# Optimization experiments

Measured on AMD Instinct MI355X. Metric: run time of the kernel, lower is better.

## Reference

```python
import jax, jax.numpy as jnp
import numpy as np

ALPHA = 0.7
NUM_HEADS = 12
NUM_KV_HEADS = 6
HEAD_DIM = 64
ROPE_BASE = 10000.0


def ternary_quantize(w):
    thr = ALPHA * jnp.mean(jnp.abs(w))
    return jnp.sign(w) * (jnp.abs(w) >= thr).astype(w.dtype)


def bitlinear(x, w):
    # forward: F.linear(x, ternary(w)) * mean(|w|)
    scale = jnp.mean(jnp.abs(w))
    qw = ternary_quantize(w)
    return (x @ qw.T) * scale


def rope_tables(seq_len, dim, dtype):
    inv_freq = 1.0 / (ROPE_BASE ** (jnp.arange(0, dim, 2, dtype=jnp.float32) / dim))
    t = jnp.arange(seq_len, dtype=jnp.float32)
    freqs = jnp.outer(t, inv_freq)            # [S, dim/2]
    emb = jnp.concatenate([freqs, freqs], -1)  # [S, dim]
    return jnp.cos(emb).astype(dtype), jnp.sin(emb).astype(dtype)


def rotate_half(x):
    x1, x2 = jnp.split(x, 2, axis=-1)
    return jnp.concatenate([-x2, x1], axis=-1)


def setup_inputs() -> dict:
    key = jax.random.key(0)
    ks = jax.random.split(key, 5)
    B, S, H = 2, 2048, 768
    return {
        "hidden_states": jax.random.normal(ks[0], (B, S, H), jnp.float32),
        "Wq": jax.random.normal(ks[1], (768, 768), jnp.float32) * 0.02,
        "Wk": jax.random.normal(ks[2], (384, 768), jnp.float32) * 0.02,
        "Wv": jax.random.normal(ks[3], (384, 768), jnp.float32) * 0.02,
        "Wo": jax.random.normal(ks[4], (768, 768), jnp.float32) * 0.02,
    }


def reference(hidden_states, Wq, Wk, Wv, Wo):
    B, S, H = hidden_states.shape
    nh, nkv, hd = NUM_HEADS, NUM_KV_HEADS, HEAD_DIM
    groups = nh // nkv

    q = bitlinear(hidden_states, Wq).reshape(B, S, nh, hd).transpose(0, 2, 1, 3)
    k = bitlinear(hidden_states, Wk).reshape(B, S, nkv, hd).transpose(0, 2, 1, 3)
    v = bitlinear(hidden_states, Wv).reshape(B, S, nkv, hd).transpose(0, 2, 1, 3)

    cos, sin = rope_tables(S, hd, hidden_states.dtype)  # [S, hd]
    cos = cos[None, None]  # [1,1,S,hd]
    sin = sin[None, None]
    q = q * cos + rotate_half(q) * sin
    k = k * cos + rotate_half(k) * sin

    # GQA: expand kv heads to full head count
    k = jnp.repeat(k, groups, axis=1)  # [B, nh, S, hd]
    v = jnp.repeat(v, groups, axis=1)

    scale = 1.0 / jnp.sqrt(jnp.asarray(hd, hidden_states.dtype))
    scores = jnp.einsum("bhsd,bhtd->bhst", q, k) * scale
    attn = jax.nn.softmax(scores, axis=-1)
    out = jnp.einsum("bhst,bhtd->bhsd", attn, v)
    out = out.transpose(0, 2, 1, 3).reshape(B, S, H)
    return bitlinear(out, Wo)
```

## Files before the change

kernel.cpp:

```cpp
#include <hip/hip_runtime.h>
#include <cmath>

typedef unsigned short u16;
typedef unsigned int u32;
typedef __bf16 bf16x2 __attribute__((ext_vector_type(2)));
typedef __bf16 bf16x8 __attribute__((ext_vector_type(8)));
typedef float f32x16 __attribute__((ext_vector_type(16)));

#define NQ (768*768)
#define NK (384*768)

__device__ __forceinline__ u16 f2bf(float f) {
  u32 u = __float_as_uint(f);
  u32 r = (u + 0x7FFFu + ((u >> 16) & 1u)) >> 16;
  return (u16)r;
}
__device__ __forceinline__ u32 packbf(float a, float b) {
#if __has_builtin(__builtin_amdgcn_cvt_pk_bf16_f32)
  bf16x2 v = __builtin_amdgcn_cvt_pk_bf16_f32(a, b);
  u32 r; __builtin_memcpy(&r, &v, 4); return r;
#else
  return (u32)f2bf(a) | ((u32)f2bf(b) << 16);
#endif
}
__device__ __forceinline__ float fexp2(float x) {
#if __has_builtin(__builtin_amdgcn_exp2f)
  return __builtin_amdgcn_exp2f(x);
#else
  return exp2f(x);
#endif
}
__device__ __forceinline__ bf16x8 ldfrag(const u16* p) { bf16x8 v; __builtin_memcpy(&v, p, 16); return v; }
__device__ __forceinline__ f32x16 mfma32_(bf16x8 a, bf16x8 b, f32x16 c) {
  return __builtin_amdgcn_mfma_f32_32x32x16_bf16(a, b, c, 0, 0, 0);
}

__device__ __forceinline__ int fidx(int r, int k) {
  return (r >> 5) * 24576 + (k >> 4) * 512 + ((r & 31) + 32 * ((k >> 3) & 1)) * 8 + (k & 7);
}
__device__ __forceinline__ int kidx(int b6kvh, int s, int d) {
  return b6kvh * 131072 + (s >> 5) * 2048 + (d >> 4) * 512 +
         ((s & 31) + 32 * ((d >> 3) & 1)) * 8 + (d & 7);
}
__device__ __forceinline__ int qidx(int b, int s, int h, int d) {
  return ((b * 64 + (s >> 5)) * 12 + h) * 2048 + (d >> 4) * 512 +
         ((s & 31) + 32 * ((d >> 3) & 1)) * 8 + (d & 7);
}
__device__ __forceinline__ int vidx(int b6kvh, int d, int p) {
  return b6kvh * 131072 + (p >> 6) * 4096 + (d >> 5) * 2048 + ((p >> 4) & 3) * 512 +
         ((d & 31) + 32 * ((p >> 3) & 1)) * 8 + (p & 7);
}

__global__ __launch_bounds__(256) void abssum_kernel(const float* __restrict__ wq, const float* __restrict__ wk,
                                                     const float* __restrict__ wv, const float* __restrict__ wo,
                                                     float* __restrict__ sums) {
  int which = blockIdx.y;
  const float* w = (which == 0) ? wq : (which == 1) ? wk : (which == 2) ? wv : wo;
  int n4 = ((which == 0 || which == 3) ? NQ : NK) >> 2;
  const float4* w4 = (const float4*)w;
  float s = 0.f;
  for (int i = blockIdx.x * blockDim.x + threadIdx.x; i < n4; i += gridDim.x * blockDim.x) {
    float4 v = w4[i];
    s += fabsf(v.x) + fabsf(v.y) + fabsf(v.z) + fabsf(v.w);
  }
  for (int off = 32; off; off >>= 1) s += __shfl_down(s, off);
  __shared__ float ls[4];
  if ((threadIdx.x & 63) == 0) ls[threadIdx.x >> 6] = s;
  __syncthreads();
  if (threadIdx.x == 0) atomicAdd(&sums[which], ls[0] + ls[1] + ls[2] + ls[3]);
}

__global__ __launch_bounds__(256) void prep_kernel(const float* __restrict__ wq, const float* __restrict__ wk,
                                                   const float* __restrict__ wv, const float* __restrict__ wo,
                                                   const float* __restrict__ sums, const float* __restrict__ x,
                                                   u16* __restrict__ qw, u16* __restrict__ woq,
                                                   u16* __restrict__ xb) {
  int i = blockIdx.x * blockDim.x + threadIdx.x;
  if (i < 221184) {
    int n = i / 96, k8 = i - n * 96;
    const float* src; float th; u16* dst; int nd;
    if (n < 768)       { src = wq + n * 768;          th = 0.7f * sums[0] * (1.f / NQ); dst = qw;  nd = n; }
    else if (n < 1152) { src = wk + (n - 768) * 768;  th = 0.7f * sums[1] * (1.f / NK); dst = qw;  nd = n; }
    else if (n < 1536) { src = wv + (n - 1152) * 768; th = 0.7f * sums[2] * (1.f / NK); dst = qw;  nd = n; }
    else               { src = wo + (n - 1536) * 768; th = 0.7f * sums[3] * (1.f / NQ); dst = woq; nd = n - 1536; }
    const float4* sp = (const float4*)(src + k8 * 8);
    float4 v0 = sp[0], v1 = sp[1];
    float e[8] = {v0.x, v0.y, v0.z, v0.w, v1.x, v1.y, v1.z, v1.w};
    u16 o[8];
#pragma unroll
    for (int j = 0; j < 8; j++)
      o[j] = f2bf((fabsf(e[j]) >= th) ? ((e[j] > 0.f) ? 1.f : -1.f) : 0.f);
    __builtin_memcpy(dst + fidx(nd, k8 * 8), o, 16);
  } else {
    int j = i - 221184;
    int m = j / 96, k8 = j - m * 96;
    const float4* xp = (const float4*)(x + m * 768 + k8 * 8);
    float4 v0 = xp[0], v1 = xp[1];
    u16 o[8] = { f2bf(v0.x), f2bf(v0.y), f2bf(v0.z), f2bf(v0.w),
                 f2bf(v1.x), f2bf(v1.y), f2bf(v1.z), f2bf(v1.w) };
    __builtin_memcpy(xb + fidx(m, k8 * 8), o, 16);
  }
}

__global__ __launch_bounds__(256, 3) void gemm_qkv_kernel(const u16* __restrict__ xb, const u16* __restrict__ qw,
                                                          const float* __restrict__ sums,
                                                          u16* __restrict__ qb, u16* __restrict__ kb,
                                                          u16* __restrict__ vT) {
  int tn = blockIdx.x, tm = blockIdx.y;
  int t = threadIdx.x, lane = t & 63, w = t >> 6, c = lane & 31, g2 = lane >> 5;
  int wm = w & 1, wn = w >> 1;
  const u16* abase = xb + (tm * 2 + wm) * 24576 + lane * 8;
  const u16* bbase0 = qw + (tn * 4 + wn * 2) * 24576 + lane * 8;
  const u16* bbase1 = bbase0 + 24576;
  f32x16 acc[2]; acc[0] = (f32x16)0.f; acc[1] = (f32x16)0.f;
  for (int kk = 0; kk < 48; kk += 4) {
#pragma unroll
    for (int ks = 0; ks < 4; ks++) {
      bf16x8 af = ldfrag(abase + (kk + ks) * 512);
      bf16x8 b0 = ldfrag(bbase0 + (kk + ks) * 512);
      bf16x8 b1 = ldfrag(bbase1 + (kk + ks) * 512);
      acc[0] = mfma32_(af, b0, acc[0]);
      acc[1] = mfma32_(af, b1, acc[1]);
    }
  }
  float sq = sums[0] * (1.f / NQ) * 0.180336880111120f;
  float sk = sums[1] * (1.f / NK);
  float sv = sums[2] * (1.f / NK);
  int mb = tm * 64 + wm * 32 + 4 * g2;
  if (tn < 9) {
    float sc = (tn < 6) ? sq : sk;
    int head = (tn < 6) ? (tn * 2 + wn) : ((tn - 6) * 2 + wn);
    float f = fexp2((float)c * -0.41524101186092029f);
#pragma unroll
    for (int r = 0; r < 16; r++) {
      int m = mb + (r & 3) + 8 * (r >> 2);
      int bb = m >> 11, s = m & 2047;
      float sn, cs; sincosf((float)s * f, &sn, &cs);
      float x1 = acc[0][r] * sc, x2 = acc[1][r] * sc;
      u16 y1 = f2bf(x1 * cs - x2 * sn);
      u16 y2 = f2bf(x2 * cs + x1 * sn);
      if (tn < 6) {
        qb[qidx(bb, s, head, c)]      = y1;
        qb[qidx(bb, s, head, c + 32)] = y2;
      } else {
        kb[kidx(bb * 6 + head, s, c)]      = y1;
        kb[kidx(bb * 6 + head, s, c + 32)] = y2;
      }
    }
  } else {
    int kvh = (tn - 9) * 2 + wn;
#pragma unroll
    for (int nb = 0; nb < 2; nb++)
#pragma unroll
      for (int r = 0; r < 16; r++) {
        int m = mb + (r & 3) + 8 * (r >> 2);
        int bb = m >> 11, s = m & 2047;
        int sp = (s & ~12) | ((s & 4) << 1) | ((s & 8) >> 1);
        vT[vidx(bb * 6 + kvh, nb * 32 + c, sp)] = f2bf(acc[nb][r] * sv);
      }
  }
}

__global__ __launch_bounds__(256, 3) void attn_kernel(const u16* __restrict__ qb, const u16* __restrict__ kb,
                                                      const u16* __restrict__ vT, u16* __restrict__ ab) {
  __shared__ float Obuf[4][32][66];
  __shared__ float Lbuf[4][32];
  int bk = blockIdx.x, qt = blockIdx.y;
  int b = bk / 6, kvh = bk % 6;
  int t = threadIdx.x, lane = t & 63, w = t >> 6, c = lane & 31, g2 = lane >> 5;
  int qn = w & 1, kh = w >> 1;

  const u16* qbase = qb + ((b * 64 + qt) * 12 + kvh * 2 + qn) * 2048;
  bf16x8 qf[4];
#pragma unroll
  for (int ks = 0; ks < 4; ks++) qf[ks] = ldfrag(qbase + ks * 512 + lane * 8);

  u32 onesw = 0x3F803F80u;
  bf16x8 ones;
  { u32 tmp[4] = {onesw, onesw, onesw, onesw}; __builtin_memcpy(&ones, tmp, 16); }

  f32x16 fz = (f32x16)0.f;
  f32x16 O[2] = {fz, fz};
  f32x16 Lacc = fz;

  const u16* Kb = kb + bk * 131072;
  const u16* Vb = vT + bk * 131072;

  for (int it = 0; it < 32; it++) {
    int kb32 = kh * 32 + it;
    const u16* kt = Kb + kb32 * 2048;
    const u16* vt = Vb + (kb32 >> 1) * 4096 + (kb32 & 1) * 1024;
    bf16x8 kf[4];
#pragma unroll
    for (int ks = 0; ks < 4; ks++) kf[ks] = ldfrag(kt + ks * 512 + lane * 8);
    bf16x8 vf[2][2];
#pragma unroll
    for (int dn = 0; dn < 2; dn++)
#pragma unroll
      for (int ksv = 0; ksv < 2; ksv++)
        vf[dn][ksv] = ldfrag(vt + dn * 2048 + ksv * 512 + lane * 8);
    f32x16 S = fz;
#pragma unroll
    for (int ks = 0; ks < 4; ks++) S = mfma32_(kf[ks], qf[ks], S);
    float e[16];
#pragma unroll
    for (int r = 0; r < 16; r++) e[r] = fexp2(S[r]);
    u32 P[8];
#pragma unroll
    for (int j = 0; j < 8; j++) P[j] = packbf(e[2 * j], e[2 * j + 1]);
    bf16x8 PA[2];
    __builtin_memcpy(&PA[0], &P[0], 16);
    __builtin_memcpy(&PA[1], &P[4], 16);
#pragma unroll
    for (int ksv = 0; ksv < 2; ksv++) {
      O[0] = mfma32_(PA[ksv], vf[0][ksv], O[0]);
      O[1] = mfma32_(PA[ksv], vf[1][ksv], O[1]);
      Lacc = mfma32_(PA[ksv], ones, Lacc);
    }
  }
  if (c == 0) {
#pragma unroll
    for (int r = 0; r < 16; r++) Lbuf[w][(r & 3) + 8 * (r >> 2) + 4 * g2] = Lacc[r];
  }
#pragma unroll
  for (int dn = 0; dn < 2; dn++)
#pragma unroll
    for (int r = 0; r < 16; r++)
      Obuf[w][(r & 3) + 8 * (r >> 2) + 4 * g2][dn * 32 + c] = O[dn][r];
  __syncthreads();
  {
    int hn = t >> 7, qq = (t >> 2) & 31, dc = (t & 3) * 16;
    float l = Lbuf[hn][qq] + Lbuf[hn + 2][qq];
    float inv = 1.f / l;
    u16 o[16];
#pragma unroll
    for (int j = 0; j < 16; j++)
      o[j] = f2bf((Obuf[hn][qq][dc + j] + Obuf[hn + 2][qq][dc + j]) * inv);
    int h = kvh * 2 + hn;
    int mg = b * 64 + qt;
    u16* dst = ab + mg * 24576 + ((h * 64 + dc) >> 4) * 512 + qq * 8;
    __builtin_memcpy(dst, o, 16);
    __builtin_memcpy(dst + 256, o + 8, 16);
  }
}

__global__ __launch_bounds__(256, 3) void gemm_out_kernel(const u16* __restrict__ ab, const u16* __restrict__ woq,
                                                          const float* __restrict__ sums, float* __restrict__ out) {
  int tn = blockIdx.x, tm = blockIdx.y;
  int t = threadIdx.x, lane = t & 63, w = t >> 6, c = lane & 31, g2 = lane >> 5;
  int wm = w & 1, wn = w >> 1;
  const u16* abase = ab + (tm * 2 + wm) * 24576 + lane * 8;
  const u16* bbase = woq + (tn * 2 + wn) * 24576 + lane * 8;
  f32x16 acc = (f32x16)0.f;
  for (int kk = 0; kk < 48; kk += 4) {
#pragma unroll
    for (int ks = 0; ks < 4; ks++) {
      bf16x8 af = ldfrag(abase + (kk + ks) * 512);
      bf16x8 bf = ldfrag(bbase + (kk + ks) * 512);
      acc = mfma32_(af, bf, acc);
    }
  }
  float so = sums[3] * (1.f / NQ);
  int mb = tm * 64 + wm * 32 + 4 * g2;
#pragma unroll
  for (int r = 0; r < 16; r++) {
    int m = mb + (r & 3) + 8 * (r >> 2);
    out[m * 768 + tn * 64 + wn * 32 + c] = acc[r] * so;
  }
}

extern "C" void kernel_launch(void* const* d_in, const int* in_sizes, int n_in,
                              void* d_out, int out_size, void* d_ws, size_t ws_size,
                              hipStream_t stream) {
  const float* x  = (const float*)d_in[0];
  const float* wq = (const float*)d_in[1];
  const float* wk = (const float*)d_in[2];
  const float* wv = (const float*)d_in[3];
  const float* wo = (const float*)d_in[4];
  float* out = (float*)d_out;
  char* ws = (char*)d_ws;

  float* sums = (float*)ws;
  u16* qw  = (u16*)(ws + 256);
  u16* woq = (u16*)(ws + 2359552);
  u16* xb  = (u16*)(ws + 3539200);
  u16* qb  = (u16*)(ws + 9830656);
  u16* kb  = (u16*)(ws + 16122112);
  u16* vT  = (u16*)(ws + 19267840);
  u16* ab  = (u16*)(ws + 22413568);

  hipMemsetAsync(sums, 0, 16, stream);
  dim3 blk(256);
  abssum_kernel<<<dim3(64, 4), blk, 0, stream>>>(wq, wk, wv, wo, sums);
  prep_kernel<<<dim3(2400), blk, 0, stream>>>(wq, wk, wv, wo, sums, x, qw, woq, xb);
  gemm_qkv_kernel<<<dim3(12, 64), blk, 0, stream>>>(xb, qw, sums, qb, kb, vT);
  attn_kernel<<<dim3(12, 64), blk, 0, stream>>>(qb, kb, vT, ab);
  gemm_out_kernel<<<dim3(12, 64), blk, 0, stream>>>(ab, woq, sums, out);
}
```

Baseline: 156.9 us.

## Retile QKV, attention, and output kernels so each wave reuses more loaded fragments

The QKV GEMM now assigns each block 128 rows by one head (4 waves along M sharing the B tiles) instead of a 64x128 tile. The output GEMM gives each wave two 32-column B tiles. Attention processes two query tiles per block so every K/V fragment load feeds twice as many MFMAs, and it replaces the ones-MFMA row-sum with per-lane sums reduced by shuffles. This cuts redundant global/L2 loads and MFMA work for the denominator. In exchange the kernels use more registers (attention launch bounds drop to 2 waves/SIMD) and launch half as many blocks.

```diff
diff --git a/kernel.cpp b/kernel.cpp
--- a/kernel.cpp
+++ b/kernel.cpp
@@ -108,9 +108,8 @@
                                                           u16* __restrict__ vT) {
   int tn = blockIdx.x, tm = blockIdx.y;
   int t = threadIdx.x, lane = t & 63, w = t >> 6, c = lane & 31, g2 = lane >> 5;
-  int wm = w & 1, wn = w >> 1;
-  const u16* abase = xb + (tm * 2 + wm) * 24576 + lane * 8;
-  const u16* bbase0 = qw + (tn * 4 + wn * 2) * 24576 + lane * 8;
+  const u16* abase = xb + (tm * 4 + w) * 24576 + lane * 8;
+  const u16* bbase0 = qw + (tn * 2) * 24576 + lane * 8;
   const u16* bbase1 = bbase0 + 24576;
   f32x16 acc[2]; acc[0] = (f32x16)0.f; acc[1] = (f32x16)0.f;
   for (int kk = 0; kk < 48; kk += 4) {
@@ -126,10 +125,10 @@
   float sq = sums[0] * (1.f / NQ) * 0.180336880111120f;
   float sk = sums[1] * (1.f / NK);
   float sv = sums[2] * (1.f / NK);
-  int mb = tm * 64 + wm * 32 + 4 * g2;
-  if (tn < 9) {
-    float sc = (tn < 6) ? sq : sk;
-    int head = (tn < 6) ? (tn * 2 + wn) : ((tn - 6) * 2 + wn);
+  int mb = tm * 128 + w * 32 + 4 * g2;
+  if (tn < 18) {
+    float sc = (tn < 12) ? sq : sk;
+    int head = (tn < 12) ? tn : (tn - 12);
     float f = fexp2((float)c * -0.41524101186092029f);
 #pragma unroll
     for (int r = 0; r < 16; r++) {
@@ -139,7 +138,7 @@
       float x1 = acc[0][r] * sc, x2 = acc[1][r] * sc;
       u16 y1 = f2bf(x1 * cs - x2 * sn);
       u16 y2 = f2bf(x2 * cs + x1 * sn);
-      if (tn < 6) {
+      if (tn < 12) {
         qb[qidx(bb, s, head, c)]      = y1;
         qb[qidx(bb, s, head, c + 32)] = y2;
       } else {
@@ -148,7 +147,7 @@
       }
     }
   } else {
-    int kvh = (tn - 9) * 2 + wn;
+    int kvh = tn - 18;
 #pragma unroll
     for (int nb = 0; nb < 2; nb++)
 #pragma unroll
@@ -161,27 +160,30 @@
   }
 }
 
-__global__ __launch_bounds__(256, 3) void attn_kernel(const u16* __restrict__ qb, const u16* __restrict__ kb,
+__global__ __launch_bounds__(256, 2) void attn_kernel(const u16* __restrict__ qb, const u16* __restrict__ kb,
                                                       const u16* __restrict__ vT, u16* __restrict__ ab) {
   __shared__ float Obuf[4][32][66];
-  __shared__ float Lbuf[4][32];
-  int bk = blockIdx.x, qt = blockIdx.y;
+  __shared__ float Lbuf[2][4][32];
+  int bk = blockIdx.x, qt2 = blockIdx.y;
   int b = bk / 6, kvh = bk % 6;
   int t = threadIdx.x, lane = t & 63, w = t >> 6, c = lane & 31, g2 = lane >> 5;
-  int qn = w & 1, kh = w >> 1;
-
-  const u16* qbase = qb + ((b * 64 + qt) * 12 + kvh * 2 + qn) * 2048;
-  bf16x8 qf[4];
-#pragma unroll
-  for (int ks = 0; ks < 4; ks++) qf[ks] = ldfrag(qbase + ks * 512 + lane * 8);
-
-  u32 onesw = 0x3F803F80u;
-  bf16x8 ones;
-  { u32 tmp[4] = {onesw, onesw, onesw, onesw}; __builtin_memcpy(&ones, tmp, 16); }
+  int hn = w & 1, kh = w >> 1;
+
+  bf16x8 qf[2][4];
+#pragma unroll
+  for (int j = 0; j < 2; j++) {
+    const u16* qbase = qb + ((b * 64 + qt2 * 2 + j) * 12 + kvh * 2 + hn) * 2048;
+#pragma unroll
+    for (int ks = 0; ks < 4; ks++) qf[j][ks] = ldfrag(qbase + ks * 512 + lane * 8);
+  }
 
   f32x16 fz = (f32x16)0.f;
-  f32x16 O[2] = {fz, fz};
-  f32x16 Lacc = fz;
+  f32x16 O[2][2] = {{fz, fz}, {fz, fz}};
+  float esum[2][16];
+#pragma unroll
+  for (int j = 0; j < 2; j++)
+#pragma unroll
+    for (int r = 0; r < 16; r++) esum[j][r] = 0.f;
 
   const u16* Kb = kb + bk * 131072;
   const u16* Vb = vT + bk * 131072;
@@ -199,45 +201,62 @@
 #pragma unroll
       for (int ksv = 0; ksv < 2; ksv++)
         vf[dn][ksv] = ldfrag(vt + dn * 2048 + ksv * 512 + lane * 8);
-    f32x16 S = fz;
-#pragma unroll
-    for (int ks = 0; ks < 4; ks++) S = mfma32_(kf[ks], qf[ks], S);
-    float e[16];
-#pragma unroll
-    for (int r = 0; r < 16; r++) e[r] = fexp2(S[r]);
-    u32 P[8];
-#pragma unroll
-    for (int j = 0; j < 8; j++) P[j] = packbf(e[2 * j], e[2 * j + 1]);
-    bf16x8 PA[2];
-    __builtin_memcpy(&PA[0], &P[0], 16);
-    __builtin_memcpy(&PA[1], &P[4], 16);
-#pragma unroll
-    for (int ksv = 0; ksv < 2; ksv++) {
-      O[0] = mfma32_(PA[ksv], vf[0][ksv], O[0]);
-      O[1] = mfma32_(PA[ksv], vf[1][ksv], O[1]);
-      Lacc = mfma32_(PA[ksv], ones, Lacc);
-    }
-  }
-  if (c == 0) {
-#pragma unroll
-    for (int r = 0; r < 16; r++) Lbuf[w][(r & 3) + 8 * (r >> 2) + 4 * g2] = Lacc[r];
-  }
-#pragma unroll
-  for (int dn = 0; dn < 2; dn++)
-#pragma unroll
-    for (int r = 0; r < 16; r++)
-      Obuf[w][(r & 3) + 8 * (r >> 2) + 4 * g2][dn * 32 + c] = O[dn][r];
-  __syncthreads();
-  {
-    int hn = t >> 7, qq = (t >> 2) & 31, dc = (t & 3) * 16;
-    float l = Lbuf[hn][qq] + Lbuf[hn + 2][qq];
+#pragma unroll
+    for (int j = 0; j < 2; j++) {
+      f32x16 S = fz;
+#pragma unroll
+      for (int ks = 0; ks < 4; ks++) S = mfma32_(kf[ks], qf[j][ks], S);
+      float e[16];
+#pragma unroll
+      for (int r = 0; r < 16; r++) {
+        e[r] = fexp2(S[r]);
+        esum[j][r] += e[r];
+      }
+      u32 P[8];
+#pragma unroll
+      for (int jj = 0; jj < 8; jj++) P[jj] = packbf(e[2 * jj], e[2 * jj + 1]);
+      bf16x8 PA[2];
+      __builtin_memcpy(&PA[0], &P[0], 16);
+      __builtin_memcpy(&PA[1], &P[4], 16);
+#pragma unroll
+      for (int ksv = 0; ksv < 2; ksv++) {
+        O[j][0] = mfma32_(PA[ksv], vf[0][ksv], O[j][0]);
+        O[j][1] = mfma32_(PA[ksv], vf[1][ksv], O[j][1]);
+      }
+    }
+  }
+#pragma unroll
+  for (int j = 0; j < 2; j++) {
+#pragma unroll
+    for (int r = 0; r < 16; r++) {
+      float v = esum[j][r];
+      v += __shfl_xor(v, 1); v += __shfl_xor(v, 2); v += __shfl_xor(v, 4);
+      v += __shfl_xor(v, 8); v += __shfl_xor(v, 16);
+      esum[j][r] = v;
+    }
+    if (c == 0) {
+#pragma unroll
+      for (int r = 0; r < 16; r++) Lbuf[j][w][(r & 3) + 8 * (r >> 2) + 4 * g2] = esum[j][r];
+    }
+  }
+#pragma unroll
+  for (int j = 0; j < 2; j++) {
+    if (j) __syncthreads();
+#pragma unroll
+    for (int dn = 0; dn < 2; dn++)
+#pragma unroll
+      for (int r = 0; r < 16; r++)
+        Obuf[w][(r & 3) + 8 * (r >> 2) + 4 * g2][dn * 32 + c] = O[j][dn][r];
+    __syncthreads();
+    int hn_c = t >> 7, qq = (t >> 2) & 31, dc = (t & 3) * 16;
+    float l = Lbuf[j][hn_c][qq] + Lbuf[j][hn_c + 2][qq];
     float inv = 1.f / l;
     u16 o[16];
 #pragma unroll
-    for (int j = 0; j < 16; j++)
-      o[j] = f2bf((Obuf[hn][qq][dc + j] + Obuf[hn + 2][qq][dc + j]) * inv);
-    int h = kvh * 2 + hn;
-    int mg = b * 64 + qt;
+    for (int jj = 0; jj < 16; jj++)
+      o[jj] = f2bf((Obuf[hn_c][qq][dc + jj] + Obuf[hn_c + 2][qq][dc + jj]) * inv);
+    int h = kvh * 2 + hn_c;
+    int mg = b * 64 + qt2 * 2 + j;
     u16* dst = ab + mg * 24576 + ((h * 64 + dc) >> 4) * 512 + qq * 8;
     __builtin_memcpy(dst, o, 16);
     __builtin_memcpy(dst + 256, o + 8, 16);
@@ -248,25 +267,29 @@
                                                           const float* __restrict__ sums, float* __restrict__ out) {
   int tn = blockIdx.x, tm = blockIdx.y;
   int t = threadIdx.x, lane = t & 63, w = t >> 6, c = lane & 31, g2 = lane >> 5;
-  int wm = w & 1, wn = w >> 1;
-  const u16* abase = ab + (tm * 2 + wm) * 24576 + lane * 8;
-  const u16* bbase = woq + (tn * 2 + wn) * 24576 + lane * 8;
-  f32x16 acc = (f32x16)0.f;
+  const u16* abase = ab + (tm * 4 + w) * 24576 + lane * 8;
+  const u16* bbase0 = woq + (tn * 2) * 24576 + lane * 8;
+  const u16* bbase1 = bbase0 + 24576;
+  f32x16 acc[2]; acc[0] = (f32x16)0.f; acc[1] = (f32x16)0.f;
   for (int kk = 0; kk < 48; kk += 4) {
 #pragma unroll
     for (int ks = 0; ks < 4; ks++) {
       bf16x8 af = ldfrag(abase + (kk + ks) * 512);
-      bf16x8 bf = ldfrag(bbase + (kk + ks) * 512);
-      acc = mfma32_(af, bf, acc);
+      bf16x8 b0 = ldfrag(bbase0 + (kk + ks) * 512);
+      bf16x8 b1 = ldfrag(bbase1 + (kk + ks) * 512);
+      acc[0] = mfma32_(af, b0, acc[0]);
+      acc[1] = mfma32_(af, b1, acc[1]);
     }
   }
   float so = sums[3] * (1.f / NQ);
-  int mb = tm * 64 + wm * 32 + 4 * g2;
-#pragma unroll
-  for (int r = 0; r < 16; r++) {
-    int m = mb + (r & 3) + 8 * (r >> 2);
-    out[m * 768 + tn * 64 + wn * 32 + c] = acc[r] * so;
-  }
+  int mb = tm * 128 + w * 32 + 4 * g2;
+#pragma unroll
+  for (int nb = 0; nb < 2; nb++)
+#pragma unroll
+    for (int r = 0; r < 16; r++) {
+      int m = mb + (r & 3) + 8 * (r >> 2);
+      out[m * 768 + tn * 64 + nb * 32 + c] = acc[nb][r] * so;
+    }
 }
 
 extern "C" void kernel_launch(void* const* d_in, const int* in_sizes, int n_in,
@@ -293,7 +316,7 @@
   dim3 blk(256);
   abssum_kernel<<<dim3(64, 4), blk, 0, stream>>>(wq, wk, wv, wo, sums);
   prep_kernel<<<dim3(2400), blk, 0, stream>>>(wq, wk, wv, wo, sums, x, qw, woq, xb);
-  gemm_qkv_kernel<<<dim3(12, 64), blk, 0, stream>>>(xb, qw, sums, qb, kb, vT);
-  attn_kernel<<<dim3(12, 64), blk, 0, stream>>>(qb, kb, vT, ab);
-  gemm_out_kernel<<<dim3(12, 64), blk, 0, stream>>>(ab, woq, sums, out);
-}
+  gemm_qkv_kernel<<<dim3(24, 32), blk, 0, stream>>>(xb, qw, sums, qb, kb, vT);
+  attn_kernel<<<dim3(12, 32), blk, 0, stream>>>(qb, kb, vT, ab);
+  gemm_out_kernel<<<dim3(12, 32), blk, 0, stream>>>(ab, woq, sums, out);
+}
```

New measurement: 168.8 us. 1.08x slower.
